# Kernel tuning notes

Hardware: AMD Instinct MI355X
Metric: run time of the kernel (lower is better)

Reference implementation:

```python
import jax, jax.numpy as jnp
import numpy as np

HEADS = 8
DIM = 512


def setup_inputs() -> dict:
    key = jax.random.key(0)
    ks = jax.random.split(key, 7)
    B, N, L, C = 2, 64, 32, DIM
    feat1 = jax.random.normal(ks[0], (B, N, L, C), dtype=jnp.float32)
    feat2 = jax.random.normal(ks[1], (B, N, L, C), dtype=jnp.float32)
    s = 1.0 / np.sqrt(C)
    Wq1 = jax.random.normal(ks[2], (C, C), dtype=jnp.float32) * s
    Wk1 = jax.random.normal(ks[3], (C, C), dtype=jnp.float32) * s
    Wq2 = jax.random.normal(ks[4], (C, C), dtype=jnp.float32) * s
    Wk2 = jax.random.normal(ks[5], (C, C), dtype=jnp.float32) * s
    tau = jnp.array(0.3, dtype=jnp.float32)
    return {"feat1": feat1, "feat2": feat2, "Wq1": Wq1, "Wk1": Wk1,
            "Wq2": Wq2, "Wk2": Wk2, "tau": tau}


def _proj_heads(x_flat, W, B, NL, H):
    # nn.Linear(bias=False): y = x @ W.T ; then split heads -> (B, H, NL, hd)
    y = jnp.einsum('btc,dc->btd', x_flat, W)
    return y.reshape(B, NL, H, -1).transpose(0, 2, 1, 3)


def _pooled_scores(Q, Kt, scale, tau, B, H, N, L):
    # scores (B,H,NL,NL) -> softmax -> view (B,H,N,L,N,L) -> amax(-1) -> mean(L) -> mean(H)
    s = jnp.einsum('bhqd,bhkd->bhqk', Q, Kt) * (scale / tau)
    s = jax.nn.softmax(s, axis=-1)
    s = s.reshape(B, H, N, L, N, L)
    s = s.max(axis=-1)          # (B,H,N,L,N)
    s = s.mean(axis=3)          # (B,H,N,N)
    return s.mean(axis=1)       # (B,N,N)


def reference(feat1, feat2, Wq1, Wk1, Wq2, Wk2, tau):
    B, N, L, C = feat1.shape
    H = HEADS
    NL = N * L
    scale = C ** (-0.5)
    f1 = feat1.reshape(B, NL, C)
    f2 = feat2.reshape(B, NL, C)
    Q1 = _proj_heads(f1, Wq1, B, NL, H)
    K1 = _proj_heads(f1, Wk1, B, NL, H)
    Q2 = _proj_heads(f2, Wq2, B, NL, H)
    K2 = _proj_heads(f2, Wk2, B, NL, H)
    c12 = _pooled_scores(Q1, K2, scale, tau, B, H, N, L)
    c21 = _pooled_scores(Q2, K1, scale, tau, B, H, N, L)
    return (c12 + c21) * 0.5
```

## Files before the change

kernel.cpp:

```cpp
#include <hip/hip_runtime.h>
#include <hip/hip_bf16.h>

#define NLQ 2048
#define CDIM 512
#define HD 64
#define NHEADS 8

typedef __attribute__((ext_vector_type(8))) short bf16x8;
typedef __attribute__((ext_vector_type(4))) float f32x4;

#define MFMA(A, B, Cc) __builtin_amdgcn_mfma_f32_16x16x32_bf16(A, B, Cc, 0, 0, 0)

__device__ __forceinline__ short f2bf(float x) {
    __hip_bfloat16 h = __float2bfloat16(x);
    return *reinterpret_cast<short*>(&h);
}

__device__ __forceinline__ int swz(int row, int colByte) {
    return ((row << 7) + colByte) ^ ((row & 7) << 4);
}

#define QK_ELEMS   8388608
#define X_ELEMS    2097152
#define W_ELEMS    262144
#define PLANE      2097152

__global__ __launch_bounds__(256) void convert_kernel(
    const float* __restrict__ f1, const float* __restrict__ f2,
    const float* __restrict__ Wq1, const float* __restrict__ Wk1,
    const float* __restrict__ Wq2, const float* __restrict__ Wk2,
    const float* __restrict__ tau, short* __restrict__ ws)
{
    short* Xb1 = ws + QK_ELEMS;
    short* Xb2 = Xb1 + X_ELEMS;
    short* Wb  = Xb2 + X_ELEMS;
    float la = 0.044194173824159216f * 1.4426950408889634f / tau[0];

    int bid = blockIdx.x;
    const float* src; short* dst; float a = 1.0f; int idx;
    if (bid < 1024)       { src = f1; dst = Xb1; idx = bid; }
    else if (bid < 2048)  { src = f2; dst = Xb2; idx = bid - 1024; }
    else {
        int wseg = (bid - 2048) >> 7;
        idx = (bid - 2048) & 127;
        src = (wseg == 0) ? Wq1 : (wseg == 1) ? Wk1 : (wseg == 2) ? Wq2 : Wk2;
        dst = Wb + wseg * W_ELEMS;
        a = (wseg == 0 || wseg == 2) ? la : 1.0f;
    }
    int off = idx * 2048 + threadIdx.x * 8;
    float4 x0 = *(const float4*)(src + off);
    float4 x1 = *(const float4*)(src + off + 4);
    bf16x8 v = { f2bf(x0.x * a), f2bf(x0.y * a), f2bf(x0.z * a), f2bf(x0.w * a),
                 f2bf(x1.x * a), f2bf(x1.y * a), f2bf(x1.z * a), f2bf(x1.w * a) };
    *(bf16x8*)(dst + off) = v;
}

__global__ __launch_bounds__(256) void proj_kernel(short* __restrict__ ws)
{
    const short* Xb1 = ws + QK_ELEMS;
    const short* Xb2 = Xb1 + X_ELEMS;
    const short* Wb  = Xb2 + X_ELEMS;
    short* qk = ws;

    int bid = blockIdx.x;
    int g  = bid >> 9;
    int mt = (bid >> 3) & 63;
    int nt = bid & 7;

    const short* X = (g < 2) ? Xb1 : Xb2;
    const short* W = Wb + g * W_ELEMS;
    short* Y = qk + g * PLANE;

    __shared__ alignas(16) short Xs[2][4096];
    __shared__ alignas(16) short Wsh[2][4096];

    int t = threadIdx.x;
    int lane = t & 63;
    int w = t >> 6;
    int m0 = mt * 64, d0 = nt * 64;

    f32x4 acc[4] = {};

    int srow = t >> 2;
    int sc   = (t & 3) * 16;
    const short* xbase = X + (m0 + srow) * CDIM + sc;
    const short* wbase = W + (d0 + srow) * CDIM + sc;

    bf16x8 xa = *(const bf16x8*)(xbase);
    bf16x8 xb = *(const bf16x8*)(xbase + 8);
    bf16x8 wa = *(const bf16x8*)(wbase);
    bf16x8 wb = *(const bf16x8*)(wbase + 8);
    *(bf16x8*)((char*)Xs[0]  + swz(srow, sc * 2))      = xa;
    *(bf16x8*)((char*)Xs[0]  + swz(srow, sc * 2 + 16)) = xb;
    *(bf16x8*)((char*)Wsh[0] + swz(srow, sc * 2))      = wa;
    *(bf16x8*)((char*)Wsh[0] + swz(srow, sc * 2 + 16)) = wb;
    __syncthreads();

    for (int kc = 0; kc < 8; ++kc) {
        int cur = kc & 1;
        if (kc < 7) {
            const short* xn = xbase + (kc + 1) * 64;
            const short* wn = wbase + (kc + 1) * 64;
            xa = *(const bf16x8*)(xn); xb = *(const bf16x8*)(xn + 8);
            wa = *(const bf16x8*)(wn); wb = *(const bf16x8*)(wn + 8);
        }
        bf16x8 af0, af1;
        {
            int rr = (w << 4) + (lane & 15);
            int cb = (lane >> 4) << 4;
            af0 = *(const bf16x8*)((const char*)Xs[cur] + swz(rr, cb));
            af1 = *(const bf16x8*)((const char*)Xs[cur] + swz(rr, cb + 64));
        }
        #pragma unroll
        for (int ns = 0; ns < 4; ++ns) {
            int rr = (ns << 4) + (lane & 15);
            int cb = (lane >> 4) << 4;
            bf16x8 b0 = *(const bf16x8*)((const char*)Wsh[cur] + swz(rr, cb));
            bf16x8 b1 = *(const bf16x8*)((const char*)Wsh[cur] + swz(rr, cb + 64));
            acc[ns] = MFMA(af0, b0, acc[ns]);
            acc[ns] = MFMA(af1, b1, acc[ns]);
        }
        if (kc < 7) {
            int nx = cur ^ 1;
            *(bf16x8*)((char*)Xs[nx]  + swz(srow, sc * 2))      = xa;
            *(bf16x8*)((char*)Xs[nx]  + swz(srow, sc * 2 + 16)) = xb;
            *(bf16x8*)((char*)Wsh[nx] + swz(srow, sc * 2))      = wa;
            *(bf16x8*)((char*)Wsh[nx] + swz(srow, sc * 2 + 16)) = wb;
        }
        __syncthreads();
    }

    #pragma unroll
    for (int ns = 0; ns < 4; ++ns) {
        #pragma unroll
        for (int j = 0; j < 4; ++j) {
            int row = m0 + (w << 4) + ((lane >> 4) << 2) + j;
            int col = d0 + (ns << 4) + (lane & 15);
            int bb = row >> 11, tl = row & 2047;
            int hh = col >> 6, hd = col & 63;
            Y[((bb * NHEADS + hh) * NLQ + tl) * HD + hd] = f2bf(acc[ns][j]);
        }
    }
}

__global__ __launch_bounds__(256) void attn_kernel(
    const short* __restrict__ qk, float* __restrict__ out)
{
    int bid = blockIdx.x;
    int qt   = bid & 31;
    int h    = (bid >> 5) & 7;
    int pair = (bid >> 8) & 1;
    int b    = bid >> 9;

    const short* Qp = qk + (pair ? 2 : 0) * PLANE;
    const short* Kp = qk + (pair ? 1 : 3) * PLANE;
    const int bh = (b * NHEADS + h) * NLQ * HD;
    const short* Q = Qp + bh;
    const short* K = Kp + bh;

    __shared__ alignas(16) short Ks[2][4096];
    __shared__ float bms[64][65];
    __shared__ float rowinv[64];
    __shared__ float partial[4][64];

    int t = threadIdx.x;
    int lane = t & 63;
    int w = t >> 6;

    bf16x8 qb0, qb1;
    {
        int row = qt * 64 + (w << 4) + (lane & 15);
        const short* qp = Q + row * HD + ((lane >> 4) << 3);
        qb0 = *(const bf16x8*)qp;
        qb1 = *(const bf16x8*)(qp + 32);
    }

    int srow = t >> 2;
    int sc   = (t & 3) * 16;
    const short* kbase = K + srow * HD + sc;

    float psum = 0.f;

    bf16x8 ka = *(const bf16x8*)(kbase);
    bf16x8 kb = *(const bf16x8*)(kbase + 8);
    *(bf16x8*)((char*)Ks[0] + swz(srow, sc * 2))      = ka;
    *(bf16x8*)((char*)Ks[0] + swz(srow, sc * 2 + 16)) = kb;
    __syncthreads();

    for (int kt = 0; kt < 32; ++kt) {
        int cur = kt & 1;
        if (kt < 31) {
            const short* kn = kbase + (kt + 1) * 64 * HD;
            ka = *(const bf16x8*)(kn);
            kb = *(const bf16x8*)(kn + 8);
        }

        f32x4 acc[4] = {};
        #pragma unroll
        for (int ks = 0; ks < 4; ++ks) {
            int rr = (ks << 4) + (lane & 15);
            int cb = (lane >> 4) << 4;
            bf16x8 a0 = *(const bf16x8*)((const char*)Ks[cur] + swz(rr, cb));
            bf16x8 a1 = *(const bf16x8*)((const char*)Ks[cur] + swz(rr, cb + 64));
            acc[ks] = MFMA(a0, qb0, acc[ks]);
            acc[ks] = MFMA(a1, qb1, acc[ks]);
        }

        float bm0 = -1e30f, bm1 = -1e30f;
        #pragma unroll
        for (int ks = 0; ks < 4; ++ks) {
            #pragma unroll
            for (int j = 0; j < 4; ++j) {
                float v = acc[ks][j];
                psum += exp2f(v);
                if (ks < 2) bm0 = fmaxf(bm0, v); else bm1 = fmaxf(bm1, v);
            }
        }
        bm0 = fmaxf(bm0, __shfl_xor(bm0, 16));
        bm0 = fmaxf(bm0, __shfl_xor(bm0, 32));
        bm1 = fmaxf(bm1, __shfl_xor(bm1, 16));
        bm1 = fmaxf(bm1, __shfl_xor(bm1, 32));
        if (lane < 16) {
            bms[2 * kt][(w << 4) + lane]     = bm0;
            bms[2 * kt + 1][(w << 4) + lane] = bm1;
        }

        if (kt < 31) {
            int nx = cur ^ 1;
            *(bf16x8*)((char*)Ks[nx] + swz(srow, sc * 2))      = ka;
            *(bf16x8*)((char*)Ks[nx] + swz(srow, sc * 2 + 16)) = kb;
        }
        __syncthreads();
    }

    psum += __shfl_xor(psum, 16);
    psum += __shfl_xor(psum, 32);
    if (lane < 16) rowinv[(w << 4) + lane] = 1.0f / psum;
    __syncthreads();

    {
        int n2 = t & 63;
        int rg = t >> 6;
        float a = 0.f;
        #pragma unroll
        for (int r = rg * 16; r < rg * 16 + 16; ++r)
            a += exp2f(bms[n2][r]) * rowinv[r];
        partial[rg][n2] = a;
    }
    __syncthreads();

    if (t < 128) {
        int n1l = t >> 6, n2 = t & 63;
        float val = (partial[2 * n1l][n2] + partial[2 * n1l + 1][n2]) * (1.0f / 512.0f);
        int n1 = qt * 2 + n1l;
        atomicAdd(&out[(b * 64 + n1) * 64 + n2], val);
    }
}

extern "C" void kernel_launch(void* const* d_in, const int* in_sizes, int n_in,
                              void* d_out, int out_size, void* d_ws, size_t ws_size,
                              hipStream_t stream) {
    const float* f1  = (const float*)d_in[0];
    const float* f2  = (const float*)d_in[1];
    const float* Wq1 = (const float*)d_in[2];
    const float* Wk1 = (const float*)d_in[3];
    const float* Wq2 = (const float*)d_in[4];
    const float* Wk2 = (const float*)d_in[5];
    const float* tau = (const float*)d_in[6];
    float* out = (float*)d_out;
    short* ws = (short*)d_ws;

    hipMemsetAsync(d_out, 0, (size_t)out_size * sizeof(float), stream);
    convert_kernel<<<dim3(2560), dim3(256), 0, stream>>>(f1, f2, Wq1, Wk1, Wq2, Wk2, tau, ws);
    proj_kernel<<<dim3(2048), dim3(256), 0, stream>>>(ws);
    attn_kernel<<<dim3(1024), dim3(256), 0, stream>>>(ws, out);
}
```

Measured before the change: 144.0 us.

## Enlarge projection tiles, split attention keys across waves, use raw v_exp

The projection GEMM moves to 128x128 tiles that fuse the Q and K weights of each input, with vectorized short4 stores, and launches four times fewer blocks. The attention kernel drops its LDS-staged K loop: each wave loads its own eighth of the keys straight from global and computes all 64 query rows, so the per-tile barrier goes away. Attention blocks are also reordered so those sharing a query tile run close together, and exp2f is replaced by raw v_exp_f32. The aim is more operand reuse and fewer barriers, at the cost of more registers per thread and unshared global K loads.

```diff
diff --git a/kernel.cpp b/kernel.cpp
--- a/kernel.cpp
+++ b/kernel.cpp
@@ -14,6 +14,12 @@
 __device__ __forceinline__ short f2bf(float x) {
     __hip_bfloat16 h = __float2bfloat16(x);
     return *reinterpret_cast<short*>(&h);
+}
+
+__device__ __forceinline__ float fast_exp2(float x) {
+    float r;
+    asm("v_exp_f32 %0, %1" : "=v"(r) : "v"(x));
+    return r;
 }
 
 __device__ __forceinline__ int swz(int row, int colByte) {
@@ -57,88 +63,109 @@
 
 __global__ __launch_bounds__(256) void proj_kernel(short* __restrict__ ws)
 {
-    const short* Xb1 = ws + QK_ELEMS;
-    const short* Xb2 = Xb1 + X_ELEMS;
-    const short* Wb  = Xb2 + X_ELEMS;
-    short* qk = ws;
-
     int bid = blockIdx.x;
-    int g  = bid >> 9;
-    int mt = (bid >> 3) & 63;
+    int gx = bid >> 8;
+    int mt = (bid >> 3) & 31;
     int nt = bid & 7;
 
-    const short* X = (g < 2) ? Xb1 : Xb2;
-    const short* W = Wb + g * W_ELEMS;
-    short* Y = qk + g * PLANE;
-
-    __shared__ alignas(16) short Xs[2][4096];
-    __shared__ alignas(16) short Wsh[2][4096];
+    const short* X   = ws + QK_ELEMS + gx * X_ELEMS;
+    const short* Wst = ws + QK_ELEMS + 2 * X_ELEMS + gx * (2 * W_ELEMS);
+    short* Yb = ws;
+
+    __shared__ alignas(16) short Alds[2][8192];
+    __shared__ alignas(16) short Blds[2][8192];
 
     int t = threadIdx.x;
     int lane = t & 63;
     int w = t >> 6;
-    int m0 = mt * 64, d0 = nt * 64;
-
-    f32x4 acc[4] = {};
-
-    int srow = t >> 2;
-    int sc   = (t & 3) * 16;
-    const short* xbase = X + (m0 + srow) * CDIM + sc;
-    const short* wbase = W + (d0 + srow) * CDIM + sc;
-
-    bf16x8 xa = *(const bf16x8*)(xbase);
-    bf16x8 xb = *(const bf16x8*)(xbase + 8);
-    bf16x8 wa = *(const bf16x8*)(wbase);
-    bf16x8 wb = *(const bf16x8*)(wbase + 8);
-    *(bf16x8*)((char*)Xs[0]  + swz(srow, sc * 2))      = xa;
-    *(bf16x8*)((char*)Xs[0]  + swz(srow, sc * 2 + 16)) = xb;
-    *(bf16x8*)((char*)Wsh[0] + swz(srow, sc * 2))      = wa;
-    *(bf16x8*)((char*)Wsh[0] + swz(srow, sc * 2 + 16)) = wb;
+    int wr = w >> 1, wc = w & 1;
+    int m0 = mt * 128, d0 = nt * 128;
+
+    int srow = t >> 1;
+    int sh = (t & 1) * 32;
+    const short* xsrc = X   + (m0 + srow) * CDIM + sh;
+    const short* wsrc = Wst + (d0 + srow) * CDIM + sh;
+
+    f32x4 acc[4][4] = {};
+
+    bf16x8 wv0 = *(const bf16x8*)(wsrc);
+    bf16x8 wv1 = *(const bf16x8*)(wsrc + 8);
+    bf16x8 wv2 = *(const bf16x8*)(wsrc + 16);
+    bf16x8 wv3 = *(const bf16x8*)(wsrc + 24);
+    bf16x8 xv0 = *(const bf16x8*)(xsrc);
+    bf16x8 xv1 = *(const bf16x8*)(xsrc + 8);
+    bf16x8 xv2 = *(const bf16x8*)(xsrc + 16);
+    bf16x8 xv3 = *(const bf16x8*)(xsrc + 24);
+    {
+        int b0 = sh * 2;
+        *(bf16x8*)((char*)Alds[0] + swz(srow, b0))      = wv0;
+        *(bf16x8*)((char*)Alds[0] + swz(srow, b0 + 16)) = wv1;
+        *(bf16x8*)((char*)Alds[0] + swz(srow, b0 + 32)) = wv2;
+        *(bf16x8*)((char*)Alds[0] + swz(srow, b0 + 48)) = wv3;
+        *(bf16x8*)((char*)Blds[0] + swz(srow, b0))      = xv0;
+        *(bf16x8*)((char*)Blds[0] + swz(srow, b0 + 16)) = xv1;
+        *(bf16x8*)((char*)Blds[0] + swz(srow, b0 + 32)) = xv2;
+        *(bf16x8*)((char*)Blds[0] + swz(srow, b0 + 48)) = xv3;
+    }
     __syncthreads();
 
     for (int kc = 0; kc < 8; ++kc) {
         int cur = kc & 1;
         if (kc < 7) {
-            const short* xn = xbase + (kc + 1) * 64;
-            const short* wn = wbase + (kc + 1) * 64;
-            xa = *(const bf16x8*)(xn); xb = *(const bf16x8*)(xn + 8);
-            wa = *(const bf16x8*)(wn); wb = *(const bf16x8*)(wn + 8);
-        }
-        bf16x8 af0, af1;
-        {
-            int rr = (w << 4) + (lane & 15);
-            int cb = (lane >> 4) << 4;
-            af0 = *(const bf16x8*)((const char*)Xs[cur] + swz(rr, cb));
-            af1 = *(const bf16x8*)((const char*)Xs[cur] + swz(rr, cb + 64));
+            const short* xn = xsrc + (kc + 1) * 64;
+            const short* wn = wsrc + (kc + 1) * 64;
+            wv0 = *(const bf16x8*)(wn);      wv1 = *(const bf16x8*)(wn + 8);
+            wv2 = *(const bf16x8*)(wn + 16); wv3 = *(const bf16x8*)(wn + 24);
+            xv0 = *(const bf16x8*)(xn);      xv1 = *(const bf16x8*)(xn + 8);
+            xv2 = *(const bf16x8*)(xn + 16); xv3 = *(const bf16x8*)(xn + 24);
+        }
+        int cb = (lane >> 4) << 4;
+        bf16x8 bfr[4][2];
+        #pragma unroll
+        for (int ms = 0; ms < 4; ++ms) {
+            int row = (wr << 6) + (ms << 4) + (lane & 15);
+            bfr[ms][0] = *(const bf16x8*)((const char*)Blds[cur] + swz(row, cb));
+            bfr[ms][1] = *(const bf16x8*)((const char*)Blds[cur] + swz(row, cb + 64));
         }
         #pragma unroll
         for (int ns = 0; ns < 4; ++ns) {
-            int rr = (ns << 4) + (lane & 15);
-            int cb = (lane >> 4) << 4;
-            bf16x8 b0 = *(const bf16x8*)((const char*)Wsh[cur] + swz(rr, cb));
-            bf16x8 b1 = *(const bf16x8*)((const char*)Wsh[cur] + swz(rr, cb + 64));
-            acc[ns] = MFMA(af0, b0, acc[ns]);
-            acc[ns] = MFMA(af1, b1, acc[ns]);
+            int arow = (wc << 6) + (ns << 4) + (lane & 15);
+            bf16x8 a0 = *(const bf16x8*)((const char*)Alds[cur] + swz(arow, cb));
+            bf16x8 a1 = *(const bf16x8*)((const char*)Alds[cur] + swz(arow, cb + 64));
+            #pragma unroll
+            for (int ms = 0; ms < 4; ++ms) {
+                acc[ms][ns] = MFMA(a0, bfr[ms][0], acc[ms][ns]);
+                acc[ms][ns] = MFMA(a1, bfr[ms][1], acc[ms][ns]);
+            }
         }
         if (kc < 7) {
             int nx = cur ^ 1;
-            *(bf16x8*)((char*)Xs[nx]  + swz(srow, sc * 2))      = xa;
-            *(bf16x8*)((char*)Xs[nx]  + swz(srow, sc * 2 + 16)) = xb;
-            *(bf16x8*)((char*)Wsh[nx] + swz(srow, sc * 2))      = wa;
-            *(bf16x8*)((char*)Wsh[nx] + swz(srow, sc * 2 + 16)) = wb;
+            int b0 = sh * 2;
+            *(bf16x8*)((char*)Alds[nx] + swz(srow, b0))      = wv0;
+            *(bf16x8*)((char*)Alds[nx] + swz(srow, b0 + 16)) = wv1;
+            *(bf16x8*)((char*)Alds[nx] + swz(srow, b0 + 32)) = wv2;
+            *(bf16x8*)((char*)Alds[nx] + swz(srow, b0 + 48)) = wv3;
+            *(bf16x8*)((char*)Blds[nx] + swz(srow, b0))      = xv0;
+            *(bf16x8*)((char*)Blds[nx] + swz(srow, b0 + 16)) = xv1;
+            *(bf16x8*)((char*)Blds[nx] + swz(srow, b0 + 32)) = xv2;
+            *(bf16x8*)((char*)Blds[nx] + swz(srow, b0 + 48)) = xv3;
         }
         __syncthreads();
     }
 
     #pragma unroll
-    for (int ns = 0; ns < 4; ++ns) {
-        #pragma unroll
-        for (int j = 0; j < 4; ++j) {
-            int row = m0 + (w << 4) + ((lane >> 4) << 2) + j;
-            int col = d0 + (ns << 4) + (lane & 15);
-            int bb = row >> 11, tl = row & 2047;
-            int hh = col >> 6, hd = col & 63;
-            Y[((bb * NHEADS + hh) * NLQ + tl) * HD + hd] = f2bf(acc[ns][j]);
+    for (int ms = 0; ms < 4; ++ms) {
+        int m = m0 + (wr << 6) + (ms << 4) + (lane & 15);
+        int bb = m >> 11, tl = m & 2047;
+        #pragma unroll
+        for (int ns = 0; ns < 4; ++ns) {
+            int d = d0 + (wc << 6) + (ns << 4) + ((lane >> 4) << 2);
+            int plane = (gx << 1) + (d >> 9);
+            int head = (d >> 6) & 7;
+            int hd = d & 63;
+            short4 v = { f2bf(acc[ms][ns][0]), f2bf(acc[ms][ns][1]),
+                         f2bf(acc[ms][ns][2]), f2bf(acc[ms][ns][3]) };
+            *(short4*)(Yb + plane * PLANE + ((bb * NHEADS + head) * NLQ + tl) * HD + hd) = v;
         }
     }
 }
@@ -147,19 +174,17 @@
     const short* __restrict__ qk, float* __restrict__ out)
 {
     int bid = blockIdx.x;
-    int qt   = bid & 31;
-    int h    = (bid >> 5) & 7;
-    int pair = (bid >> 8) & 1;
-    int b    = bid >> 9;
-
-    const short* Qp = qk + (pair ? 2 : 0) * PLANE;
-    const short* Kp = qk + (pair ? 1 : 3) * PLANE;
-    const int bh = (b * NHEADS + h) * NLQ * HD;
-    const short* Q = Qp + bh;
-    const short* K = Kp + bh;
-
-    __shared__ alignas(16) short Ks[2][4096];
+    int combo = bid & 31;
+    int qt = bid >> 5;
+    int h    = combo & 7;
+    int pair = (combo >> 3) & 1;
+    int b    = combo >> 4;
+
+    const short* Q = qk + (pair ? 2 : 0) * PLANE + (b * NHEADS + h) * NLQ * HD;
+    const short* K = qk + (pair ? 1 : 3) * PLANE + (b * NHEADS + h) * NLQ * HD;
+
     __shared__ float bms[64][65];
+    __shared__ float psums[4][64];
     __shared__ float rowinv[64];
     __shared__ float partial[4][64];
 
@@ -167,75 +192,79 @@
     int lane = t & 63;
     int w = t >> 6;
 
-    bf16x8 qb0, qb1;
-    {
-        int row = qt * 64 + (w << 4) + (lane & 15);
+    bf16x8 qb[4][2];
+    #pragma unroll
+    for (int qs = 0; qs < 4; ++qs) {
+        int row = qt * 64 + (qs << 4) + (lane & 15);
         const short* qp = Q + row * HD + ((lane >> 4) << 3);
-        qb0 = *(const bf16x8*)qp;
-        qb1 = *(const bf16x8*)(qp + 32);
-    }
-
-    int srow = t >> 2;
-    int sc   = (t & 3) * 16;
-    const short* kbase = K + srow * HD + sc;
-
-    float psum = 0.f;
-
-    bf16x8 ka = *(const bf16x8*)(kbase);
-    bf16x8 kb = *(const bf16x8*)(kbase + 8);
-    *(bf16x8*)((char*)Ks[0] + swz(srow, sc * 2))      = ka;
-    *(bf16x8*)((char*)Ks[0] + swz(srow, sc * 2 + 16)) = kb;
-    __syncthreads();
-
-    for (int kt = 0; kt < 32; ++kt) {
-        int cur = kt & 1;
-        if (kt < 31) {
-            const short* kn = kbase + (kt + 1) * 64 * HD;
-            ka = *(const bf16x8*)(kn);
-            kb = *(const bf16x8*)(kn + 8);
-        }
-
-        f32x4 acc[4] = {};
+        qb[qs][0] = *(const bf16x8*)qp;
+        qb[qs][1] = *(const bf16x8*)(qp + 32);
+    }
+
+    float ps[4] = {0.f, 0.f, 0.f, 0.f};
+
+    for (int i = 0; i < 8; ++i) {
+        int kt = (w << 3) + i;
+        int k0 = kt << 6;
+
+        bf16x8 af[4][2];
         #pragma unroll
         for (int ks = 0; ks < 4; ++ks) {
-            int rr = (ks << 4) + (lane & 15);
-            int cb = (lane >> 4) << 4;
-            bf16x8 a0 = *(const bf16x8*)((const char*)Ks[cur] + swz(rr, cb));
-            bf16x8 a1 = *(const bf16x8*)((const char*)Ks[cur] + swz(rr, cb + 64));
-            acc[ks] = MFMA(a0, qb0, acc[ks]);
-            acc[ks] = MFMA(a1, qb1, acc[ks]);
-        }
-
-        float bm0 = -1e30f, bm1 = -1e30f;
+            const short* kp = K + (k0 + (ks << 4) + (lane & 15)) * HD + ((lane >> 4) << 3);
+            af[ks][0] = *(const bf16x8*)kp;
+            af[ks][1] = *(const bf16x8*)(kp + 32);
+        }
+
+        f32x4 acc[4][4] = {};
         #pragma unroll
         for (int ks = 0; ks < 4; ++ks) {
             #pragma unroll
-            for (int j = 0; j < 4; ++j) {
-                float v = acc[ks][j];
-                psum += exp2f(v);
-                if (ks < 2) bm0 = fmaxf(bm0, v); else bm1 = fmaxf(bm1, v);
+            for (int qs = 0; qs < 4; ++qs) {
+                acc[ks][qs] = MFMA(af[ks][0], qb[qs][0], acc[ks][qs]);
+                acc[ks][qs] = MFMA(af[ks][1], qb[qs][1], acc[ks][qs]);
             }
         }
-        bm0 = fmaxf(bm0, __shfl_xor(bm0, 16));
-        bm0 = fmaxf(bm0, __shfl_xor(bm0, 32));
-        bm1 = fmaxf(bm1, __shfl_xor(bm1, 16));
-        bm1 = fmaxf(bm1, __shfl_xor(bm1, 32));
-        if (lane < 16) {
-            bms[2 * kt][(w << 4) + lane]     = bm0;
-            bms[2 * kt + 1][(w << 4) + lane] = bm1;
-        }
-
-        if (kt < 31) {
-            int nx = cur ^ 1;
-            *(bf16x8*)((char*)Ks[nx] + swz(srow, sc * 2))      = ka;
-            *(bf16x8*)((char*)Ks[nx] + swz(srow, sc * 2 + 16)) = kb;
-        }
-        __syncthreads();
-    }
-
-    psum += __shfl_xor(psum, 16);
-    psum += __shfl_xor(psum, 32);
-    if (lane < 16) rowinv[(w << 4) + lane] = 1.0f / psum;
+
+        #pragma unroll
+        for (int qs = 0; qs < 4; ++qs) {
+            float g0 = (fast_exp2(acc[0][qs][0]) + fast_exp2(acc[0][qs][1]))
+                     + (fast_exp2(acc[0][qs][2]) + fast_exp2(acc[0][qs][3]));
+            float g1 = (fast_exp2(acc[1][qs][0]) + fast_exp2(acc[1][qs][1]))
+                     + (fast_exp2(acc[1][qs][2]) + fast_exp2(acc[1][qs][3]));
+            float g2 = (fast_exp2(acc[2][qs][0]) + fast_exp2(acc[2][qs][1]))
+                     + (fast_exp2(acc[2][qs][2]) + fast_exp2(acc[2][qs][3]));
+            float g3 = (fast_exp2(acc[3][qs][0]) + fast_exp2(acc[3][qs][1]))
+                     + (fast_exp2(acc[3][qs][2]) + fast_exp2(acc[3][qs][3]));
+            ps[qs] += (g0 + g1) + (g2 + g3);
+
+            float a0 = fmaxf(fmaxf(acc[0][qs][0], acc[0][qs][1]), acc[0][qs][2]);
+            float a1 = fmaxf(fmaxf(acc[0][qs][3], acc[1][qs][0]), acc[1][qs][1]);
+            float bm0 = fmaxf(fmaxf(a0, a1), fmaxf(acc[1][qs][2], acc[1][qs][3]));
+            float a2 = fmaxf(fmaxf(acc[2][qs][0], acc[2][qs][1]), acc[2][qs][2]);
+            float a3 = fmaxf(fmaxf(acc[2][qs][3], acc[3][qs][0]), acc[3][qs][1]);
+            float bm1 = fmaxf(fmaxf(a2, a3), fmaxf(acc[3][qs][2], acc[3][qs][3]));
+
+            bm0 = fmaxf(bm0, __shfl_xor(bm0, 16));
+            bm0 = fmaxf(bm0, __shfl_xor(bm0, 32));
+            bm1 = fmaxf(bm1, __shfl_xor(bm1, 16));
+            bm1 = fmaxf(bm1, __shfl_xor(bm1, 32));
+            if (lane < 16) {
+                bms[2 * kt][(qs << 4) + lane]     = bm0;
+                bms[2 * kt + 1][(qs << 4) + lane] = bm1;
+            }
+        }
+    }
+
+    #pragma unroll
+    for (int qs = 0; qs < 4; ++qs) {
+        float s = ps[qs];
+        s += __shfl_xor(s, 16);
+        s += __shfl_xor(s, 32);
+        if (lane < 16) psums[w][(qs << 4) + lane] = s;
+    }
+    __syncthreads();
+    if (t < 64) rowinv[t] = 1.0f /
+        ((psums[0][t] + psums[1][t]) + (psums[2][t] + psums[3][t]));
     __syncthreads();
 
     {
@@ -244,7 +273,7 @@
         float a = 0.f;
         #pragma unroll
         for (int r = rg * 16; r < rg * 16 + 16; ++r)
-            a += exp2f(bms[n2][r]) * rowinv[r];
+            a += fast_exp2(bms[n2][r]) * rowinv[r];
         partial[rg][n2] = a;
     }
     __syncthreads();
@@ -252,8 +281,7 @@
     if (t < 128) {
         int n1l = t >> 6, n2 = t & 63;
         float val = (partial[2 * n1l][n2] + partial[2 * n1l + 1][n2]) * (1.0f / 512.0f);
-        int n1 = qt * 2 + n1l;
-        atomicAdd(&out[(b * 64 + n1) * 64 + n2], val);
+        atomicAdd(&out[(b * 64 + qt * 2 + n1l) * 64 + n2], val);
     }
 }
 
@@ -272,6 +300,6 @@
 
     hipMemsetAsync(d_out, 0, (size_t)out_size * sizeof(float), stream);
     convert_kernel<<<dim3(2560), dim3(256), 0, stream>>>(f1, f2, Wq1, Wk1, Wq2, Wk2, tau, ws);
-    proj_kernel<<<dim3(2048), dim3(256), 0, stream>>>(ws);
+    proj_kernel<<<dim3(512), dim3(256), 0, stream>>>(ws);
     attn_kernel<<<dim3(1024), dim3(256), 0, stream>>>(ws, out);
 }
```

New measurement: 134.9 us. 6.3% less time.
